# Optimization experiments

Measured on AMD Instinct MI355X. Metric: run time of the kernel, lower is better.

## Reference

```python
import jax, jax.numpy as jnp
import numpy as np

N_NODES = 50000
N_EDGES = 800000
NFEAT, NHID, NCLASS = 256, 64, 40


def setup_inputs() -> dict:
    key = jax.random.key(0)
    ks = jax.random.split(key, 8)
    x = jax.random.normal(ks[0], (N_NODES, NFEAT), dtype=jnp.float32)
    W1 = jax.random.normal(ks[1], (NFEAT, NHID), dtype=jnp.float32) * (1.0 / np.sqrt(NFEAT))
    b1 = jax.random.normal(ks[2], (NHID,), dtype=jnp.float32) * 0.01
    W2 = jax.random.normal(ks[3], (NHID, NCLASS), dtype=jnp.float32) * (1.0 / np.sqrt(NHID))
    b2 = jax.random.normal(ks[4], (NCLASS,), dtype=jnp.float32) * 0.01
    edge_weight = jax.random.uniform(ks[5], (N_EDGES,), dtype=jnp.float32)
    edge_src = jax.random.randint(ks[6], (N_EDGES,), 0, N_NODES)
    edge_dst = jax.random.randint(ks[7], (N_EDGES,), 0, N_NODES)
    return {"x": x, "W1": W1, "b1": b1, "W2": W2, "b2": b2,
            "edge_weight": edge_weight, "edge_src": edge_src, "edge_dst": edge_dst}


def reference(x, W1, b1, W2, b2, edge_weight, edge_src, edge_dst):
    n = x.shape[0]

    def spmm(h):  # sparse adj @ h via gather + weighted segment-sum
        msgs = h[edge_src] * edge_weight[:, None]  # [E, d]
        return jax.ops.segment_sum(msgs, edge_dst, num_segments=n)

    # gc1: adj @ (x @ W1) + b1, then relu (dropout is identity in eval mode)
    h = jax.nn.relu(spmm(x @ W1) + b1)
    # gc2: adj @ (h @ W2) + b2
    logits = spmm(h @ W2) + b2
    return (logits, jax.nn.log_softmax(logits, axis=1))
```

## Files before the change

### kernel.cpp

```cpp
#include <hip/hip_runtime.h>
#include <math.h>

#define N_NODES 50000
#define N_EDGES 800000
#define NFEAT 256
#define NHID 64
#define NCLASS 40
#define NPAD_ROWS 50048
#define NPB 16
#define NB  3125
#define BIN_EPB 8192

typedef __attribute__((ext_vector_type(8))) short bf16x8;
typedef __attribute__((ext_vector_type(4))) float f32x4;

__device__ __forceinline__ ushort f2bf(float f) {
    unsigned u = __float_as_uint(f);
    u += 0x7FFF + ((u >> 16) & 1);
    return (ushort)(u >> 16);
}
__device__ __forceinline__ float bf2f(ushort us) {
    return __uint_as_float(((unsigned)us) << 16);
}


__global__ __launch_bounds__(256) void k_bhist(const int* __restrict__ edst,
                                               int* __restrict__ bcnt) {
    __shared__ int lh[NB];
    int tid = threadIdx.x;
    for (int i = tid; i < NB; i += 256) lh[i] = 0;
    __syncthreads();
    int base = blockIdx.x * 4096;
    #pragma unroll
    for (int k = 0; k < 4096; k += 256) {
        int e = base + k + tid;
        if (e < N_EDGES) atomicAdd(&lh[edst[e] >> 4], 1);
    }
    __syncthreads();
    for (int i = tid; i < NB; i += 256) {
        int c = lh[i];
        if (c) atomicAdd(&bcnt[i], c);
    }
}

__global__ void k_bscan(const int* __restrict__ bcnt, int* __restrict__ bstart,
                        int* __restrict__ bcur, int* __restrict__ cursor) {
    int i = blockIdx.x * 256 + threadIdx.x;
    int lane = threadIdx.x & 63;
    int c = (i < NB) ? bcnt[i] : 0;
    int incl = c;
    #pragma unroll
    for (int off = 1; off < 64; off <<= 1) {
        int n = __shfl_up(incl, off);
        if (lane >= off) incl += n;
    }
    int total = __shfl(incl, 63);
    int base = 0;
    if (lane == 0) base = atomicAdd(cursor, total);
    base = __shfl(base, 0);
    if (i < NB) {
        int s = base + incl - c;
        bstart[i] = s;
        bcur[i] = s;
    }
}

__global__ __launch_bounds__(1024) void k_bin(const int* __restrict__ esrc,
                                              const int* __restrict__ edst,
                                              const float* __restrict__ ewt,
                                              int* __restrict__ bcur,
                                              int2* __restrict__ binned) {
    __shared__ int lcnt[NB];
    __shared__ int lbase[NB];
    int tid = threadIdx.x;
    for (int i = tid; i < NB; i += 1024) lcnt[i] = 0;
    __syncthreads();
    int base = blockIdx.x * BIN_EPB;
    #pragma unroll
    for (int k = 0; k < BIN_EPB; k += 1024) {
        int e = base + k + tid;
        if (e < N_EDGES) atomicAdd(&lcnt[edst[e] >> 4], 1);
    }
    __syncthreads();
    for (int i = tid; i < NB; i += 1024) {
        int c = lcnt[i];
        lbase[i] = c ? atomicAdd(&bcur[i], c) : 0;
        lcnt[i] = 0;
    }
    __syncthreads();
    #pragma unroll
    for (int k = 0; k < BIN_EPB; k += 1024) {
        int e = base + k + tid;
        if (e < N_EDGES) {
            int d = edst[e];
            int b = d >> 4;
            int pos = lbase[b] + atomicAdd(&lcnt[b], 1);
            binned[pos] = make_int2(esrc[e] | ((d & 15) << 16), __float_as_int(ewt[e]));
        }
    }
}


__global__ void k_prep(const float* __restrict__ W1, const float* __restrict__ W2,
                       ushort* __restrict__ W1f, ushort* __restrict__ W2f) {
    int idx = blockIdx.x * 256 + threadIdx.x;
    if (idx < 2048) {
        int lane = idx & 63, ctks = idx >> 6;
        int ks = ctks & 7, ct = ctks >> 3;
        int col = ct * 16 + (lane & 15);
        int r0 = ks * 32 + (lane >> 4) * 8;
        bf16x8 frag;
        #pragma unroll
        for (int j = 0; j < 8; ++j) frag[j] = (short)f2bf(W1[(r0 + j) * NHID + col]);
        *(bf16x8*)&W1f[(size_t)idx * 8] = frag;
    } else if (idx < 2048 + 384) {
        int i2 = idx - 2048;
        int lane = i2 & 63, ctks = i2 >> 6;
        int ks = ctks & 1, ct = ctks >> 1;
        int col = ct * 16 + (lane & 15);
        int r0 = ks * 32 + (lane >> 4) * 8;
        bf16x8 frag;
        #pragma unroll
        for (int j = 0; j < 8; ++j)
            frag[j] = (short)((col < NCLASS) ? f2bf(W2[(r0 + j) * NCLASS + col]) : 0);
        *(bf16x8*)&W2f[(size_t)i2 * 8] = frag;
    }
}


__global__ __launch_bounds__(256) void k_gemm1(const float* __restrict__ x,
                                               const ushort* __restrict__ W1f,
                                               ushort* __restrict__ xW1b) {
    __shared__ ushort sX[16 * 256];
    int tid = threadIdx.x;
    int w = tid >> 6, lane = tid & 63;
    int row0 = blockIdx.x * 16;

    bf16x8 Bf[8];
    #pragma unroll
    for (int ks = 0; ks < 8; ++ks)
        Bf[ks] = *(const bf16x8*)&W1f[(size_t)((w * 8 + ks) * 64 + lane) * 8];

    {
        int row = tid & 15;
        int colbase = (tid >> 4) * 16;
        const float* xp = x + (size_t)(row0 + row) * NFEAT + colbase;
        #pragma unroll
        for (int c2 = 0; c2 < 2; ++c2) {
            float4 v0 = *(const float4*)(xp + c2 * 8);
            float4 v1 = *(const float4*)(xp + c2 * 8 + 4);
            bf16x8 fr;
            fr[0] = (short)f2bf(v0.x); fr[1] = (short)f2bf(v0.y);
            fr[2] = (short)f2bf(v0.z); fr[3] = (short)f2bf(v0.w);
            fr[4] = (short)f2bf(v1.x); fr[5] = (short)f2bf(v1.y);
            fr[6] = (short)f2bf(v1.z); fr[7] = (short)f2bf(v1.w);
            int chunk = colbase / 8 + c2;
            *(bf16x8*)&sX[row * 256 + ((chunk ^ (row & 7)) * 8)] = fr;
        }
    }
    __syncthreads();

    f32x4 acc = {0.f, 0.f, 0.f, 0.f};
    int arow = lane & 15;
    #pragma unroll
    for (int ks = 0; ks < 8; ++ks) {
        int chunk = ks * 4 + (lane >> 4);
        bf16x8 Af = *(const bf16x8*)&sX[arow * 256 + ((chunk ^ (arow & 7)) * 8)];
        acc = __builtin_amdgcn_mfma_f32_16x16x32_bf16(Af, Bf[ks], acc, 0, 0, 0);
    }
    int col = w * 16 + (lane & 15);
    int rbase = row0 + (lane >> 4) * 4;
    #pragma unroll
    for (int r = 0; r < 4; ++r)
        xW1b[(size_t)(rbase + r) * NHID + col] = f2bf(acc[r]);
}

__global__ __launch_bounds__(256) void k_spmm1b(const ushort* __restrict__ xW1b,
                                                const int* __restrict__ bstart,
                                                const int* __restrict__ bcur,
                                                const int2* __restrict__ binned,
                                                const float* __restrict__ b1,
                                                ushort* __restrict__ h_b) {
    __shared__ float accs[4][NPB * NHID];
    int wv = threadIdx.x >> 6, lane = threadIdx.x & 63;
    int b = blockIdx.x;
    float* acc = accs[wv];
    #pragma unroll
    for (int n = 0; n < NPB; ++n) acc[n * NHID + lane] = 0.f;

    int s = bstart[b], e = bcur[b];
    int len = e - s;
    int q = (len + 3) >> 2;
    int j = s + wv * q;
    int je = min(j + q, e);
    for (; j + 8 <= je; j += 8) {
        int2 p[8];
        #pragma unroll
        for (int k = 0; k < 8; ++k) p[k] = binned[j + k];
        float g[8];
        #pragma unroll
        for (int k = 0; k < 8; ++k)
            g[k] = bf2f(xW1b[(p[k].x & 0xFFFF) * NHID + lane]);
        #pragma unroll
        for (int k = 0; k < 8; ++k)
            acc[(p[k].x >> 16) * NHID + lane] += __int_as_float(p[k].y) * g[k];
    }
    for (; j < je; ++j) {
        int2 p0 = binned[j];
        float g0 = bf2f(xW1b[(p0.x & 0xFFFF) * NHID + lane]);
        acc[(p0.x >> 16) * NHID + lane] += __int_as_float(p0.y) * g0;
    }
    __syncthreads();

    float bias = b1[lane];
    #pragma unroll
    for (int i = 0; i < 4; ++i) {
        int n = wv * 4 + i;
        float v = accs[0][n * NHID + lane] + accs[1][n * NHID + lane]
                + accs[2][n * NHID + lane] + accs[3][n * NHID + lane] + bias;
        h_b[(size_t)(b * NPB + n) * NHID + lane] = f2bf(v > 0.f ? v : 0.f);
    }
}


__global__ __launch_bounds__(256) void k_gemm2(const ushort* __restrict__ h_b,
                                               const ushort* __restrict__ W2f,
                                               ushort* __restrict__ hW2b) {
    int tid = threadIdx.x;
    int w = tid >> 6, lane = tid & 63;
    int row0 = blockIdx.x * 64 + w * 16;

    f32x4 acc[3] = {{0.f,0.f,0.f,0.f},{0.f,0.f,0.f,0.f},{0.f,0.f,0.f,0.f}};
    #pragma unroll
    for (int ks = 0; ks < 2; ++ks) {
        bf16x8 Af = *(const bf16x8*)&h_b[(size_t)(row0 + (lane & 15)) * NHID
                                         + ks * 32 + (lane >> 4) * 8];
        #pragma unroll
        for (int ct = 0; ct < 3; ++ct) {
            bf16x8 Bf = *(const bf16x8*)&W2f[(size_t)((ct * 2 + ks) * 64 + lane) * 8];
            acc[ct] = __builtin_amdgcn_mfma_f32_16x16x32_bf16(Af, Bf, acc[ct], 0, 0, 0);
        }
    }
    int rbase = row0 + (lane >> 4) * 4;
    #pragma unroll
    for (int ct = 0; ct < 3; ++ct) {
        int col = ct * 16 + (lane & 15);
        if (col < NCLASS) {
            #pragma unroll
            for (int r = 0; r < 4; ++r) {
                int row = rbase + r;
                if (row < N_NODES)
                    hW2b[(size_t)row * NCLASS + col] = f2bf(acc[ct][r]);
            }
        }
    }
}

__global__ __launch_bounds__(256) void k_spmm2b(const ushort* __restrict__ hW2b,
                                                const int* __restrict__ bstart,
                                                const int* __restrict__ bcur,
                                                const int2* __restrict__ binned,
                                                const float* __restrict__ b2,
                                                float* __restrict__ out) {
    __shared__ float accs[4][NPB * 64];
    int wv = threadIdx.x >> 6, lane = threadIdx.x & 63;
    int b = blockIdx.x;
    float* acc = accs[wv];
    int lf = lane < NCLASS ? lane : 0;
    #pragma unroll
    for (int n = 0; n < NPB; ++n) acc[n * 64 + lane] = 0.f;

    int s = bstart[b], e = bcur[b];
    int len = e - s;
    int q = (len + 3) >> 2;
    int j = s + wv * q;
    int je = min(j + q, e);
    for (; j + 8 <= je; j += 8) {
        int2 p[8];
        #pragma unroll
        for (int k = 0; k < 8; ++k) p[k] = binned[j + k];
        float g[8];
        #pragma unroll
        for (int k = 0; k < 8; ++k)
            g[k] = bf2f(hW2b[(p[k].x & 0xFFFF) * NCLASS + lf]);
        #pragma unroll
        for (int k = 0; k < 8; ++k)
            acc[(p[k].x >> 16) * 64 + lane] += __int_as_float(p[k].y) * g[k];
    }
    for (; j < je; ++j) {
        int2 p0 = binned[j];
        float g0 = bf2f(hW2b[(p0.x & 0xFFFF) * NCLASS + lf]);
        acc[(p0.x >> 16) * 64 + lane] += __int_as_float(p0.y) * g0;
    }
    __syncthreads();

    float bias = (lane < NCLASS) ? b2[lane] : 0.f;
    #pragma unroll
    for (int i = 0; i < 4; ++i) {
        int n = wv * 4 + i;
        float vs = accs[0][n * 64 + lane] + accs[1][n * 64 + lane]
                 + accs[2][n * 64 + lane] + accs[3][n * 64 + lane];
        float v = (lane < NCLASS) ? (vs + bias) : -INFINITY;
        float m = v;
        #pragma unroll
        for (int off = 32; off; off >>= 1) m = fmaxf(m, __shfl_xor(m, off));
        float ex = (lane < NCLASS) ? __expf(v - m) : 0.f;
        float ssum = ex;
        #pragma unroll
        for (int off = 32; off; off >>= 1) ssum += __shfl_xor(ssum, off);
        float ls = __logf(ssum);
        if (lane < NCLASS) {
            int node = b * NPB + n;
            out[(size_t)node * NCLASS + lane] = v;
            out[(size_t)N_NODES * NCLASS + (size_t)node * NCLASS + lane] = v - m - ls;
        }
    }
}


extern "C" void kernel_launch(void* const* d_in, const int* in_sizes, int n_in,
                              void* d_out, int out_size, void* d_ws, size_t ws_size,
                              hipStream_t stream) {
    const float* x    = (const float*)d_in[0];
    const float* W1   = (const float*)d_in[1];
    const float* b1   = (const float*)d_in[2];
    const float* W2   = (const float*)d_in[3];
    const float* b2   = (const float*)d_in[4];
    const float* ewt  = (const float*)d_in[5];
    const int*   esrc = (const int*)d_in[6];
    const int*   edst = (const int*)d_in[7];
    float* out = (float*)d_out;

    char* p = (char*)d_ws;
    ushort* xW1b = (ushort*)p;   p += (size_t)N_NODES * NHID * 2;
    ushort* h_b  = (ushort*)p;   p += (size_t)NPAD_ROWS * NHID * 2;
    ushort* hW2b = (ushort*)p;   p += (size_t)N_NODES * NCLASS * 2;
    int2*   binned = (int2*)p;   p += (size_t)N_EDGES * 8;
    ushort* W1f  = (ushort*)p;   p += 2048 * 8 * 2;
    ushort* W2f  = (ushort*)p;   p += 384 * 8 * 2;
    int* bcnt    = (int*)p;      p += NB * 4;
    int* cursor  = (int*)p;      p += 4;
    int* bstart  = (int*)p;      p += NB * 4;
    int* bcur    = (int*)p;      p += NB * 4;

    hipMemsetAsync(bcnt, 0, (NB + 1) * sizeof(int), stream);

    k_bhist<<<(N_EDGES + 4095) / 4096, 256, 0, stream>>>(edst, bcnt);
    k_bscan<<<(NB + 255) / 256, 256, 0, stream>>>(bcnt, bstart, bcur, cursor);
    k_bin<<<(N_EDGES + BIN_EPB - 1) / BIN_EPB, 1024, 0, stream>>>(esrc, edst, ewt, bcur, binned);
    k_prep<<<10, 256, 0, stream>>>(W1, W2, W1f, W2f);

    k_gemm1<<<N_NODES / 16, 256, 0, stream>>>(x, W1f, xW1b);
    k_spmm1b<<<NB, 256, 0, stream>>>(xW1b, bstart, bcur, binned, b1, h_b);
    k_gemm2<<<NPAD_ROWS / 64, 256, 0, stream>>>(h_b, W2f, hW2b);
    k_spmm2b<<<NB, 256, 0, stream>>>(hW2b, bstart, bcur, binned, b2, out);
}
```

Baseline: 212.0 us.

## Reorder layer-2 as aggregate-then-transform and fuse GEMM2 into SpMM, merge prep into hist

Layer 2 now aggregates h (64-wide) over edges first, then applies W2 with MFMA inside the same block before bias and log_softmax. This removes the separate gemm2 kernel and its hW2b round trip through memory. The cost is a wider per-edge gather (64 instead of 40 columns). Weight fragment prep is also folded into the histogram kernel as extra blocks, which saves one launch. The accumulator row stride is padded to 68 to reduce LDS bank conflicts.

```diff
diff --git a/kernel.cpp b/kernel.cpp
--- a/kernel.cpp
+++ b/kernel.cpp
@@ -6,10 +6,11 @@
 #define NFEAT 256
 #define NHID 64
 #define NCLASS 40
-#define NPAD_ROWS 50048
 #define NPB 16
 #define NB  3125
 #define BIN_EPB 8192
+#define NHB 196
+#define ACC2S 68
 
 typedef __attribute__((ext_vector_type(8))) short bf16x8;
 typedef __attribute__((ext_vector_type(4))) float f32x4;
@@ -23,11 +24,39 @@
     return __uint_as_float(((unsigned)us) << 16);
 }
 
-
-__global__ __launch_bounds__(256) void k_bhist(const int* __restrict__ edst,
-                                               int* __restrict__ bcnt) {
+__global__ __launch_bounds__(256) void k_histprep(const int* __restrict__ edst,
+                                                  int* __restrict__ bcnt,
+                                                  const float* __restrict__ W1,
+                                                  const float* __restrict__ W2,
+                                                  ushort* __restrict__ W1f,
+                                                  ushort* __restrict__ W2f) {
     __shared__ int lh[NB];
     int tid = threadIdx.x;
+    if (blockIdx.x >= NHB) {
+        int idx = (blockIdx.x - NHB) * 256 + tid;
+        if (idx < 2048) {
+            int lane = idx & 63, ctks = idx >> 6;
+            int ks = ctks & 7, ct = ctks >> 3;
+            int col = ct * 16 + (lane & 15);
+            int r0 = ks * 32 + (lane >> 4) * 8;
+            bf16x8 frag;
+            #pragma unroll
+            for (int j = 0; j < 8; ++j) frag[j] = (short)f2bf(W1[(r0 + j) * NHID + col]);
+            *(bf16x8*)&W1f[(size_t)idx * 8] = frag;
+        } else if (idx < 2048 + 384) {
+            int i2 = idx - 2048;
+            int lane = i2 & 63, ctks = i2 >> 6;
+            int ks = ctks & 1, ct = ctks >> 1;
+            int col = ct * 16 + (lane & 15);
+            int r0 = ks * 32 + (lane >> 4) * 8;
+            bf16x8 frag;
+            #pragma unroll
+            for (int j = 0; j < 8; ++j)
+                frag[j] = (short)((col < NCLASS) ? f2bf(W2[(r0 + j) * NCLASS + col]) : 0);
+            *(bf16x8*)&W2f[(size_t)i2 * 8] = frag;
+        }
+        return;
+    }
     for (int i = tid; i < NB; i += 256) lh[i] = 0;
     __syncthreads();
     int base = blockIdx.x * 4096;
@@ -97,33 +126,6 @@
             int pos = lbase[b] + atomicAdd(&lcnt[b], 1);
             binned[pos] = make_int2(esrc[e] | ((d & 15) << 16), __float_as_int(ewt[e]));
         }
-    }
-}
-
-
-__global__ void k_prep(const float* __restrict__ W1, const float* __restrict__ W2,
-                       ushort* __restrict__ W1f, ushort* __restrict__ W2f) {
-    int idx = blockIdx.x * 256 + threadIdx.x;
-    if (idx < 2048) {
-        int lane = idx & 63, ctks = idx >> 6;
-        int ks = ctks & 7, ct = ctks >> 3;
-        int col = ct * 16 + (lane & 15);
-        int r0 = ks * 32 + (lane >> 4) * 8;
-        bf16x8 frag;
-        #pragma unroll
-        for (int j = 0; j < 8; ++j) frag[j] = (short)f2bf(W1[(r0 + j) * NHID + col]);
-        *(bf16x8*)&W1f[(size_t)idx * 8] = frag;
-    } else if (idx < 2048 + 384) {
-        int i2 = idx - 2048;
-        int lane = i2 & 63, ctks = i2 >> 6;
-        int ks = ctks & 1, ct = ctks >> 1;
-        int col = ct * 16 + (lane & 15);
-        int r0 = ks * 32 + (lane >> 4) * 8;
-        bf16x8 frag;
-        #pragma unroll
-        for (int j = 0; j < 8; ++j)
-            frag[j] = (short)((col < NCLASS) ? f2bf(W2[(r0 + j) * NCLASS + col]) : 0);
-        *(bf16x8*)&W2f[(size_t)i2 * 8] = frag;
     }
 }
 
@@ -222,53 +224,19 @@
     }
 }
 
-
-__global__ __launch_bounds__(256) void k_gemm2(const ushort* __restrict__ h_b,
-                                               const ushort* __restrict__ W2f,
-                                               ushort* __restrict__ hW2b) {
-    int tid = threadIdx.x;
-    int w = tid >> 6, lane = tid & 63;
-    int row0 = blockIdx.x * 64 + w * 16;
-
-    f32x4 acc[3] = {{0.f,0.f,0.f,0.f},{0.f,0.f,0.f,0.f},{0.f,0.f,0.f,0.f}};
-    #pragma unroll
-    for (int ks = 0; ks < 2; ++ks) {
-        bf16x8 Af = *(const bf16x8*)&h_b[(size_t)(row0 + (lane & 15)) * NHID
-                                         + ks * 32 + (lane >> 4) * 8];
-        #pragma unroll
-        for (int ct = 0; ct < 3; ++ct) {
-            bf16x8 Bf = *(const bf16x8*)&W2f[(size_t)((ct * 2 + ks) * 64 + lane) * 8];
-            acc[ct] = __builtin_amdgcn_mfma_f32_16x16x32_bf16(Af, Bf, acc[ct], 0, 0, 0);
-        }
-    }
-    int rbase = row0 + (lane >> 4) * 4;
-    #pragma unroll
-    for (int ct = 0; ct < 3; ++ct) {
-        int col = ct * 16 + (lane & 15);
-        if (col < NCLASS) {
-            #pragma unroll
-            for (int r = 0; r < 4; ++r) {
-                int row = rbase + r;
-                if (row < N_NODES)
-                    hW2b[(size_t)row * NCLASS + col] = f2bf(acc[ct][r]);
-            }
-        }
-    }
-}
-
-__global__ __launch_bounds__(256) void k_spmm2b(const ushort* __restrict__ hW2b,
+__global__ __launch_bounds__(256) void k_spmm2f(const ushort* __restrict__ h_b,
                                                 const int* __restrict__ bstart,
                                                 const int* __restrict__ bcur,
                                                 const int2* __restrict__ binned,
+                                                const ushort* __restrict__ W2f,
                                                 const float* __restrict__ b2,
                                                 float* __restrict__ out) {
-    __shared__ float accs[4][NPB * 64];
+    __shared__ float accs[4][NPB * ACC2S];
     int wv = threadIdx.x >> 6, lane = threadIdx.x & 63;
     int b = blockIdx.x;
     float* acc = accs[wv];
-    int lf = lane < NCLASS ? lane : 0;
-    #pragma unroll
-    for (int n = 0; n < NPB; ++n) acc[n * 64 + lane] = 0.f;
+    #pragma unroll
+    for (int n = 0; n < NPB; ++n) acc[n * ACC2S + lane] = 0.f;
 
     int s = bstart[b], e = bcur[b];
     int len = e - s;
@@ -282,38 +250,64 @@
         float g[8];
         #pragma unroll
         for (int k = 0; k < 8; ++k)
-            g[k] = bf2f(hW2b[(p[k].x & 0xFFFF) * NCLASS + lf]);
+            g[k] = bf2f(h_b[(p[k].x & 0xFFFF) * NHID + lane]);
         #pragma unroll
         for (int k = 0; k < 8; ++k)
-            acc[(p[k].x >> 16) * 64 + lane] += __int_as_float(p[k].y) * g[k];
+            acc[(p[k].x >> 16) * ACC2S + lane] += __int_as_float(p[k].y) * g[k];
     }
     for (; j < je; ++j) {
         int2 p0 = binned[j];
-        float g0 = bf2f(hW2b[(p0.x & 0xFFFF) * NCLASS + lf]);
-        acc[(p0.x >> 16) * 64 + lane] += __int_as_float(p0.y) * g0;
-    }
-    __syncthreads();
-
-    float bias = (lane < NCLASS) ? b2[lane] : 0.f;
+        float g0 = bf2f(h_b[(p0.x & 0xFFFF) * NHID + lane]);
+        acc[(p0.x >> 16) * ACC2S + lane] += __int_as_float(p0.y) * g0;
+    }
+    __syncthreads();
+
+    for (int i = threadIdx.x; i < NPB * 64; i += 256) {
+        int idx = (i >> 6) * ACC2S + (i & 63);
+        accs[0][idx] = accs[0][idx] + accs[1][idx] + accs[2][idx] + accs[3][idx];
+    }
+    __syncthreads();
+    if (wv != 0) return;
+
+    bf16x8 Af[2];
+    #pragma unroll
+    for (int ks = 0; ks < 2; ++ks) {
+        const float* ap = &accs[0][(lane & 15) * ACC2S + ks * 32 + (lane >> 4) * 8];
+        #pragma unroll
+        for (int jj = 0; jj < 8; ++jj) Af[ks][jj] = (short)f2bf(ap[jj]);
+    }
+    f32x4 cv[3] = {{0.f,0.f,0.f,0.f},{0.f,0.f,0.f,0.f},{0.f,0.f,0.f,0.f}};
+    #pragma unroll
+    for (int ct = 0; ct < 3; ++ct) {
+        #pragma unroll
+        for (int ks = 0; ks < 2; ++ks) {
+            bf16x8 Bf = *(const bf16x8*)&W2f[(size_t)((ct * 2 + ks) * 64 + lane) * 8];
+            cv[ct] = __builtin_amdgcn_mfma_f32_16x16x32_bf16(Af[ks], Bf, cv[ct], 0, 0, 0);
+        }
+    }
+    int colg = lane & 15;
+    int g = lane >> 4;
+    float bc0 = b2[colg];
+    float bc1 = b2[16 + colg];
+    float bc2 = (colg < 8) ? b2[32 + colg] : 0.f;
     #pragma unroll
     for (int i = 0; i < 4; ++i) {
-        int n = wv * 4 + i;
-        float vs = accs[0][n * 64 + lane] + accs[1][n * 64 + lane]
-                 + accs[2][n * 64 + lane] + accs[3][n * 64 + lane];
-        float v = (lane < NCLASS) ? (vs + bias) : -INFINITY;
-        float m = v;
-        #pragma unroll
-        for (int off = 32; off; off >>= 1) m = fmaxf(m, __shfl_xor(m, off));
-        float ex = (lane < NCLASS) ? __expf(v - m) : 0.f;
-        float ssum = ex;
-        #pragma unroll
-        for (int off = 32; off; off >>= 1) ssum += __shfl_xor(ssum, off);
-        float ls = __logf(ssum);
-        if (lane < NCLASS) {
-            int node = b * NPB + n;
-            out[(size_t)node * NCLASS + lane] = v;
-            out[(size_t)N_NODES * NCLASS + (size_t)node * NCLASS + lane] = v - m - ls;
-        }
+        int node = b * NPB + g * 4 + i;
+        float v0 = cv[0][i] + bc0;
+        float v1 = cv[1][i] + bc1;
+        float v2 = (colg < 8) ? (cv[2][i] + bc2) : -INFINITY;
+        float m = fmaxf(fmaxf(v0, v1), v2);
+        #pragma unroll
+        for (int off = 1; off < 16; off <<= 1) m = fmaxf(m, __shfl_xor(m, off));
+        float ex = __expf(v0 - m) + __expf(v1 - m) + ((colg < 8) ? __expf(v2 - m) : 0.f);
+        #pragma unroll
+        for (int off = 1; off < 16; off <<= 1) ex += __shfl_xor(ex, off);
+        float ls = __logf(ex) + m;
+        float* o0 = out + (size_t)node * NCLASS;
+        float* o1 = o0 + (size_t)N_NODES * NCLASS;
+        o0[colg] = v0;            o1[colg] = v0 - ls;
+        o0[16 + colg] = v1;       o1[16 + colg] = v1 - ls;
+        if (colg < 8) { o0[32 + colg] = v2;  o1[32 + colg] = v2 - ls; }
     }
 }
 
@@ -333,8 +327,7 @@
 
     char* p = (char*)d_ws;
     ushort* xW1b = (ushort*)p;   p += (size_t)N_NODES * NHID * 2;
-    ushort* h_b  = (ushort*)p;   p += (size_t)NPAD_ROWS * NHID * 2;
-    ushort* hW2b = (ushort*)p;   p += (size_t)N_NODES * NCLASS * 2;
+    ushort* h_b  = (ushort*)p;   p += (size_t)N_NODES * NHID * 2;
     int2*   binned = (int2*)p;   p += (size_t)N_EDGES * 8;
     ushort* W1f  = (ushort*)p;   p += 2048 * 8 * 2;
     ushort* W2f  = (ushort*)p;   p += 384 * 8 * 2;
@@ -345,13 +338,11 @@
 
     hipMemsetAsync(bcnt, 0, (NB + 1) * sizeof(int), stream);
 
-    k_bhist<<<(N_EDGES + 4095) / 4096, 256, 0, stream>>>(edst, bcnt);
+    k_histprep<<<NHB + 10, 256, 0, stream>>>(edst, bcnt, W1, W2, W1f, W2f);
     k_bscan<<<(NB + 255) / 256, 256, 0, stream>>>(bcnt, bstart, bcur, cursor);
     k_bin<<<(N_EDGES + BIN_EPB - 1) / BIN_EPB, 1024, 0, stream>>>(esrc, edst, ewt, bcur, binned);
-    k_prep<<<10, 256, 0, stream>>>(W1, W2, W1f, W2f);
 
     k_gemm1<<<N_NODES / 16, 256, 0, stream>>>(x, W1f, xW1b);
     k_spmm1b<<<NB, 256, 0, stream>>>(xW1b, bstart, bcur, binned, b1, h_b);
-    k_gemm2<<<NPAD_ROWS / 64, 256, 0, stream>>>(h_b, W2f, hW2b);
-    k_spmm2b<<<NB, 256, 0, stream>>>(hW2b, bstart, bcur, binned, b2, out);
-}
+    k_spmm2f<<<NB, 256, 0, stream>>>(h_b, bstart, bcur, binned, W2f, b2, out);
+}
```

Measured after the change: 200.5 us. 5.4% less time.
